# Kernel optimization log

Hardware: AMD Instinct MI355X
Metric: run time of the kernel (lower is better)

## Reference

```python
import jax, jax.numpy as jnp
import numpy as np

HEADS = 16
DIM_HEAD = 64
SCALE = DIM_HEAD ** -0.5


def setup_inputs() -> dict:
    key = jax.random.key(0)
    k1, k2, k3, k4 = jax.random.split(key, 4)
    b, n, dim = 4, 4096, 1024
    dim_inner = HEADS * DIM_HEAD
    x = jax.random.normal(k1, (b, n, dim), dtype=jnp.float32)
    W_qkv = jax.random.normal(k2, (dim, dim_inner * 3), dtype=jnp.float32) * 0.02
    agent_tokens = jax.random.normal(k3, (HEADS, 128, DIM_HEAD), dtype=jnp.float32) * 0.02
    W_out = jax.random.normal(k4, (dim_inner, dim), dtype=jnp.float32) * 0.02
    return {"x": x, "W_qkv": W_qkv, "agent_tokens": agent_tokens, "W_out": W_out}


def reference(x, W_qkv, agent_tokens, W_out):
    b, n, _ = x.shape
    h, m, d = agent_tokens.shape
    # qkv projection: b n (3 h d) -> 3, b, h, n, d
    qkv = (x @ W_qkv).reshape(b, n, 3, h, d).transpose(2, 0, 3, 1, 4)
    q, k, v = qkv[0], qkv[1], qkv[2]
    a = agent_tokens * SCALE  # h m d, broadcast over batch
    qa_sim = jnp.einsum('bhid,hjd->bhij', q, a)   # b h n m
    ak_sim = jnp.einsum('hid,bhjd->bhij', a, k)   # b h m n
    qa_attn = jax.nn.softmax(qa_sim, axis=-1)
    ak_attn = jax.nn.softmax(ak_sim, axis=-1)
    out = jnp.einsum('bhij,bhjd->bhid', ak_attn, v)    # b h m d
    out = jnp.einsum('bhij,bhjd->bhid', qa_attn, out)  # b h n d
    out = out.transpose(0, 2, 1, 3).reshape(b, n, h * d)
    return out @ W_out
```

## Files before the change

### kernel.cpp

```cpp
#include <hip/hip_runtime.h>

typedef __bf16 bf16x8 __attribute__((ext_vector_type(8)));
typedef float f32x4 __attribute__((ext_vector_type(4)));
typedef unsigned short ushort8 __attribute__((ext_vector_type(8)));
typedef unsigned short u16;

#define MFMA16(a, b, c) __builtin_amdgcn_mfma_f32_16x16x32_bf16(a, b, c, 0, 0, 0)
#define FENCE() __builtin_amdgcn_sched_barrier(0)
#define BARRIER() do { FENCE(); __builtin_amdgcn_s_barrier(); FENCE(); } while (0)
#define VMCNT(n) do { asm volatile("s_waitcnt vmcnt(" #n ")"); FENCE(); } while (0)

__device__ __forceinline__ u16 f2bf(float v) {
  unsigned int u = __builtin_bit_cast(unsigned int, v);
  u += 0x7fffu + ((u >> 16) & 1u);
  return (u16)(u >> 16);
}

__device__ __forceinline__ void gload16(const u16* g, u16* l) {
  __builtin_amdgcn_global_load_lds((__attribute__((address_space(1))) void*)(g),
                                   (__attribute__((address_space(3))) void*)(l), 16, 0, 0);
}

__global__ __launch_bounds__(256) void prep(const float* __restrict__ x, u16* __restrict__ x_bf,
                                            const float* __restrict__ Wqkv, u16* __restrict__ wqkvT,
                                            const float* __restrict__ Wout, u16* __restrict__ woutT,
                                            const float* __restrict__ agent, u16* __restrict__ a_bf) {
  __shared__ float tile[64][65];
  int bid = blockIdx.x;
  int t = threadIdx.x;
  if (bid < 8192) {
    size_t i = (size_t)bid * 256 + t;
    const float4* p = (const float4*)x + i * 2;
    float4 a = p[0], b = p[1];
    ushort8 o;
    o[0] = f2bf(a.x); o[1] = f2bf(a.y); o[2] = f2bf(a.z); o[3] = f2bf(a.w);
    o[4] = f2bf(b.x); o[5] = f2bf(b.y); o[6] = f2bf(b.z); o[7] = f2bf(b.w);
    *((ushort8*)x_bf + i) = o;
    return;
  }
  if (bid >= 9216) {
    int i = (bid - 9216) * 256 + t;
    a_bf[i] = f2bf(agent[i] * 0.125f);
    return;
  }
  const float* W; u16* WT; int K = 1024, N; int b2;
  if (bid < 8960) { W = Wqkv; WT = wqkvT; N = 3072; b2 = bid - 8192; }
  else            { W = Wout; WT = woutT; N = 1024; b2 = bid - 8960; }
  int nt = N >> 6;
  int kt = b2 / nt, nti = b2 - kt * nt;
  int k0 = kt << 6, n0 = nti << 6;
  int r = t >> 4, c4 = (t & 15) << 2;
#pragma unroll
  for (int j = 0; j < 4; ++j) {
    float4 v = *(const float4*)&W[(size_t)(k0 + j * 16 + r) * N + n0 + c4];
    tile[j * 16 + r][c4] = v.x; tile[j * 16 + r][c4 + 1] = v.y;
    tile[j * 16 + r][c4 + 2] = v.z; tile[j * 16 + r][c4 + 3] = v.w;
  }
  __syncthreads();
  int rn = t >> 2, cs = (t & 3) << 4;
  ushort8 o0, o1;
#pragma unroll
  for (int e = 0; e < 8; ++e) { o0[e] = f2bf(tile[cs + e][rn]); o1[e] = f2bf(tile[cs + 8 + e][rn]); }
  u16* dst = WT + (size_t)(n0 + rn) * K + k0 + cs;
  *(ushort8*)dst = o0;
  *(ushort8*)(dst + 8) = o1;
}

template <int MODE>
__global__ __launch_bounds__(512, 2) void gemm256(const u16* __restrict__ A, const u16* __restrict__ BT,
                                                  int M, int N, int K,
                                                  u16* __restrict__ qb, u16* __restrict__ kb,
                                                  u16* __restrict__ vt, float* __restrict__ outf) {
  extern __shared__ char smem[];
  const int NT = K >> 5;
  int ntiles = N >> 8;
  int nwg = (M >> 8) * ntiles;
  int bid = blockIdx.x;
  int wg = (bid & 7) * (nwg >> 3) + (bid >> 3);
  int tm = wg / ntiles, tn = wg - tm * ntiles;
  int rb = tm << 8, cb = tn << 8;
  int t = threadIdx.x;
  int w = t >> 6, lane = t & 63, li = lane & 15, lg = lane >> 4;
  int wr = w >> 2, wc = w & 3;

  const u16* srcA[2];
  const u16* srcB[2];
#pragma unroll
  for (int j = 0; j < 2; ++j) {
    int D = j * 8192 + t * 16;
    int L = D ^ (((D >> 7) & 3) << 4);
    int row = L >> 6, inb = L & 63;
    srcA[j] = A + (size_t)(rb + row) * K + (inb >> 1);
    srcB[j] = BT + (size_t)(cb + row) * K + (inb >> 1);
  }
#define STAGE_A(slot, kt) do { \
    gload16(srcA[0] + (kt) * 32, (u16*)(smem + (slot) * 32768 + t * 16)); \
    gload16(srcA[1] + (kt) * 32, (u16*)(smem + (slot) * 32768 + 8192 + t * 16)); } while (0)
#define STAGE_B(slot, kt) do { \
    gload16(srcB[0] + (kt) * 32, (u16*)(smem + (slot) * 32768 + 16384 + t * 16)); \
    gload16(srcB[1] + (kt) * 32, (u16*)(smem + (slot) * 32768 + 24576 + t * 16)); } while (0)

  int offA[8], offB[4];
#pragma unroll
  for (int m8 = 0; m8 < 8; ++m8) {
    int row = wr * 128 + m8 * 16 + li;
    int L = row * 64 + lg * 16;
    offA[m8] = L ^ (((L >> 7) & 3) << 4);
  }
#pragma unroll
  for (int n = 0; n < 4; ++n) {
    int row = wc * 64 + n * 16 + li;
    int L = row * 64 + lg * 16;
    offB[n] = 16384 + (L ^ (((L >> 7) & 3) << 4));
  }

  f32x4 acc[8][4];
#pragma unroll
  for (int m = 0; m < 8; ++m)
#pragma unroll
    for (int n = 0; n < 4; ++n) acc[m][n] = (f32x4){0.f, 0.f, 0.f, 0.f};

  bf16x8 aF[4], aS[4], b0[4], b1[4];

#define RD_A_LO(sb, d) do { d[0] = *(const bf16x8*)((sb) + offA[0]); d[1] = *(const bf16x8*)((sb) + offA[1]); \
                            d[2] = *(const bf16x8*)((sb) + offA[2]); d[3] = *(const bf16x8*)((sb) + offA[3]); } while (0)
#define RD_A_HI(sb, d) do { d[0] = *(const bf16x8*)((sb) + offA[4]); d[1] = *(const bf16x8*)((sb) + offA[5]); \
                            d[2] = *(const bf16x8*)((sb) + offA[6]); d[3] = *(const bf16x8*)((sb) + offA[7]); } while (0)
#define RD_B(sb, d)    do { d[0] = *(const bf16x8*)((sb) + offB[0]); d[1] = *(const bf16x8*)((sb) + offB[1]); \
                            d[2] = *(const bf16x8*)((sb) + offB[2]); d[3] = *(const bf16x8*)((sb) + offB[3]); } while (0)

#define PH_EVEN(t, BC, STG) do { \
    BARRIER(); \
    { char* sb_ = smem + ((t) & 3) * 32768; RD_A_HI(sb_, aS); } \
    if (STG) STAGE_A(((t) + 3) & 3, (t) + 3); \
    FENCE(); \
    __builtin_amdgcn_s_setprio(1); \
    _Pragma("unroll") for (int m = 0; m < 4; ++m) \
      _Pragma("unroll") for (int n = 0; n < 4; ++n) acc[m][n] = MFMA16(aF[m], BC[n], acc[m][n]); \
    __builtin_amdgcn_s_setprio(0); \
  } while (0)

#define PH_ODD(t, BC, BN, STG, RDNEXT, WAITOP) do { \
    WAITOP; \
    BARRIER(); \
    if (RDNEXT) { char* sb_ = smem + (((t) + 1) & 3) * 32768; RD_A_LO(sb_, aF); RD_B(sb_, BN); } \
    if (STG) STAGE_B(((t) + 3) & 3, (t) + 3); \
    FENCE(); \
    __builtin_amdgcn_s_setprio(1); \
    _Pragma("unroll") for (int m = 0; m < 4; ++m) \
      _Pragma("unroll") for (int n = 0; n < 4; ++n) acc[4 + m][n] = MFMA16(aS[m], BC[n], acc[4 + m][n]); \
    __builtin_amdgcn_s_setprio(0); \
  } while (0)

#define TILE(t, BC, BN, STG, RDNEXT, WAITOP) do { \
    PH_EVEN(t, BC, STG); \
    PH_ODD(t, BC, BN, STG, RDNEXT, WAITOP); \
  } while (0)

  STAGE_A(0, 0); STAGE_B(0, 0);
  STAGE_A(1, 1); STAGE_B(1, 1);
  STAGE_A(2, 2); STAGE_B(2, 2);
  VMCNT(8);
  BARRIER();
  RD_A_LO(smem, aF); RD_B(smem, b0);

  for (int tt = 0; tt <= NT - 6; tt += 2) {
    TILE(tt,     b0, b1, 1, 1, VMCNT(6));
    TILE(tt + 1, b1, b0, 1, 1, VMCNT(6));
  }
  TILE(NT - 4, b0, b1, 1, 1, VMCNT(6));
  TILE(NT - 3, b1, b0, 0, 1, VMCNT(4));
  TILE(NT - 2, b0, b1, 0, 1, VMCNT(0));
  TILE(NT - 1, b1, b0, 0, 0, ((void)0));

  if (MODE == 0) {
    int col0 = cb + wc * 64;
    int s = col0 >> 10;
    int hh = (col0 >> 6) & 15;
    if (s < 2) {
      u16* dst = (s == 0) ? qb : kb;
#pragma unroll
      for (int m = 0; m < 8; ++m) {
        int rbase = rb + wr * 128 + m * 16 + lg * 4;
#pragma unroll
        for (int r = 0; r < 4; ++r) {
          int rr = rbase + r;
          size_t o = (((size_t)(rr >> 12) * 16 + hh) * 4096 + (rr & 4095)) * 64;
#pragma unroll
          for (int n = 0; n < 4; ++n) dst[o + n * 16 + li] = f2bf(acc[m][n][r]);
        }
      }
    } else {
      BARRIER();
#pragma unroll
      for (int m = 0; m < 8; ++m) {
        int rl = wr * 128 + m * 16 + lg * 4;
#pragma unroll
        for (int n = 0; n < 4; ++n) {
          int colL = wc * 64 + n * 16 + li;
          unsigned int lo = (unsigned int)f2bf(acc[m][n][0]) | ((unsigned int)f2bf(acc[m][n][1]) << 16);
          unsigned int hi = (unsigned int)f2bf(acc[m][n][2]) | ((unsigned int)f2bf(acc[m][n][3]) << 16);
          int byte = (colL * 512 + rl * 2) ^ ((colL & 7) << 4);
          *(uint2*)(smem + byte) = make_uint2(lo, hi);
        }
      }
      BARRIER();
      int bb = rb >> 12, nnb = rb & 4095;
      int hh0b = (cb >> 6) & 15;
#pragma unroll
      for (int it = 0; it < 16; ++it) {
        int c = (it & 3) * 64 + w * 8 + (lane >> 3);
        int k = (it >> 2) * 8 + (lane & 7);
        int kk = (k & ~7) | ((k & 7) ^ (c & 7));
        uint4 v = *(const uint4*)(smem + c * 512 + kk * 16);
        size_t off = (((size_t)bb * 16 + hh0b + (c >> 6)) * 64 + (c & 63)) * 4096 + nnb + k * 8;
        *(uint4*)(vt + off) = v;
      }
    }
  } else {
#pragma unroll
    for (int m = 0; m < 8; ++m) {
#pragma unroll
      for (int r = 0; r < 4; ++r) {
        float* po = outf + (size_t)(rb + wr * 128 + m * 16 + lg * 4 + r) * N + cb + wc * 64;
#pragma unroll
        for (int n = 0; n < 4; ++n) po[n * 16 + li] = acc[m][n][r];
      }
    }
  }
#undef TILE
#undef PH_ODD
#undef PH_EVEN
#undef RD_A_LO
#undef RD_A_HI
#undef RD_B
#undef STAGE_A
#undef STAGE_B
}

__global__ __launch_bounds__(256) void ak_flash(const u16* __restrict__ kb, const u16* __restrict__ vt,
                                                const u16* __restrict__ ab,
                                                float* __restrict__ pO, float* __restrict__ pM,
                                                float* __restrict__ pL) {
  __shared__ u16 p_lds[128][136];
  int bid = blockIdx.x;
  int s = bid & 7;
  int bh = bid >> 3;
  int h = bh & 15;
  int t = threadIdx.x, w = t >> 6, l = t & 63, lg = l >> 4, li = l & 15;
  int jb = w * 32;

  bf16x8 afr[2][2];
#pragma unroll
  for (int jt = 0; jt < 2; ++jt)
#pragma unroll
    for (int kk = 0; kk < 2; ++kk)
      afr[jt][kk] = *(const bf16x8*)&ab[(size_t)(h * 128 + jb + jt * 16 + li) * 64 + kk * 32 + lg * 8];

  f32x4 O[2][4];
  float mrow[2][4], lrow[2][4];
#pragma unroll
  for (int jt = 0; jt < 2; ++jt) {
#pragma unroll
    for (int dt = 0; dt < 4; ++dt) O[jt][dt] = (f32x4){0.f, 0.f, 0.f, 0.f};
#pragma unroll
    for (int r = 0; r < 4; ++r) { mrow[jt][r] = -1e30f; lrow[jt][r] = 0.f; }
  }
  const u16* kbase = kb + (size_t)bh * 4096 * 64;
  const u16* vbase = vt + (size_t)bh * 64 * 4096;

  for (int c = 0; c < 4; ++c) {
    int i0 = s * 512 + c * 128;
    f32x4 sf[2][8];
#pragma unroll
    for (int jt = 0; jt < 2; ++jt)
#pragma unroll
      for (int it = 0; it < 8; ++it) sf[jt][it] = (f32x4){0.f, 0.f, 0.f, 0.f};
#pragma unroll
    for (int it = 0; it < 8; ++it)
#pragma unroll
      for (int kk = 0; kk < 2; ++kk) {
        bf16x8 bfr = *(const bf16x8*)&kbase[(size_t)(i0 + it * 16 + li) * 64 + kk * 32 + lg * 8];
        sf[0][it] = MFMA16(afr[0][kk], bfr, sf[0][it]);
        sf[1][it] = MFMA16(afr[1][kk], bfr, sf[1][it]);
      }
#pragma unroll
    for (int jt = 0; jt < 2; ++jt)
#pragma unroll
      for (int r = 0; r < 4; ++r) {
        float cm = sf[jt][0][r];
#pragma unroll
        for (int it = 1; it < 8; ++it) cm = fmaxf(cm, sf[jt][it][r]);
#pragma unroll
        for (int off = 1; off < 16; off <<= 1) cm = fmaxf(cm, __shfl_xor(cm, off));
        float mold = mrow[jt][r];
        float mnew = fmaxf(mold, cm);
        float scale = __expf(mold - mnew);
        float ss = 0.f;
#pragma unroll
        for (int it = 0; it < 8; ++it) {
          float p = __expf(sf[jt][it][r] - mnew);
          sf[jt][it][r] = p;
          ss += p;
        }
#pragma unroll
        for (int off = 1; off < 16; off <<= 1) ss += __shfl_xor(ss, off);
        lrow[jt][r] = lrow[jt][r] * scale + ss;
        mrow[jt][r] = mnew;
#pragma unroll
        for (int dt = 0; dt < 4; ++dt) O[jt][dt][r] *= scale;
      }
#pragma unroll
    for (int jt = 0; jt < 2; ++jt)
#pragma unroll
      for (int it = 0; it < 8; ++it)
#pragma unroll
        for (int r = 0; r < 4; ++r)
          p_lds[jb + jt * 16 + lg * 4 + r][it * 16 + li] = f2bf(sf[jt][it][r]);
#pragma unroll
    for (int ks = 0; ks < 4; ++ks) {
      bf16x8 pa0 = *(const bf16x8*)&p_lds[jb + li][ks * 32 + lg * 8];
      bf16x8 pa1 = *(const bf16x8*)&p_lds[jb + 16 + li][ks * 32 + lg * 8];
#pragma unroll
      for (int dt = 0; dt < 4; ++dt) {
        bf16x8 bv = *(const bf16x8*)&vbase[(size_t)(dt * 16 + li) * 4096 + i0 + ks * 32 + lg * 8];
        O[0][dt] = MFMA16(pa0, bv, O[0][dt]);
        O[1][dt] = MFMA16(pa1, bv, O[1][dt]);
      }
    }
  }
  size_t pb = ((size_t)bh * 8 + s) * 128;
#pragma unroll
  for (int jt = 0; jt < 2; ++jt)
#pragma unroll
    for (int dt = 0; dt < 4; ++dt)
#pragma unroll
      for (int r = 0; r < 4; ++r) {
        int j = jb + jt * 16 + lg * 4 + r;
        pO[(pb + j) * 64 + dt * 16 + li] = O[jt][dt][r];
      }
  if (li == 0) {
#pragma unroll
    for (int jt = 0; jt < 2; ++jt)
#pragma unroll
      for (int r = 0; r < 4; ++r) {
        int j = jb + jt * 16 + lg * 4 + r;
        pM[pb + j] = mrow[jt][r];
        pL[pb + j] = lrow[jt][r];
      }
  }
}

__global__ __launch_bounds__(128) void ak_combine(const float* __restrict__ pO, const float* __restrict__ pM,
                                                  const float* __restrict__ pL, u16* __restrict__ out1t) {
  int bh = blockIdx.x >> 3, dc = blockIdx.x & 7;
  int j = threadIdx.x;
  float ms[8], wv[8];
  float M = -1e30f;
#pragma unroll
  for (int s = 0; s < 8; ++s) { ms[s] = pM[((size_t)bh * 8 + s) * 128 + j]; M = fmaxf(M, ms[s]); }
  float L = 0.f;
#pragma unroll
  for (int s = 0; s < 8; ++s) { wv[s] = __expf(ms[s] - M); L += wv[s] * pL[((size_t)bh * 8 + s) * 128 + j]; }
  float inv = 1.f / L;
  float4 A = {0.f, 0.f, 0.f, 0.f}, B = {0.f, 0.f, 0.f, 0.f};
#pragma unroll
  for (int s = 0; s < 8; ++s) {
    const float4* p = (const float4*)&pO[(((size_t)bh * 8 + s) * 128 + j) * 64 + dc * 8];
    float4 x = p[0], y = p[1];
    A.x += wv[s] * x.x; A.y += wv[s] * x.y; A.z += wv[s] * x.z; A.w += wv[s] * x.w;
    B.x += wv[s] * y.x; B.y += wv[s] * y.y; B.z += wv[s] * y.z; B.w += wv[s] * y.w;
  }
  size_t ob = ((size_t)bh * 64 + dc * 8) * 128 + j;
  out1t[ob + 0 * 128] = f2bf(A.x * inv);
  out1t[ob + 1 * 128] = f2bf(A.y * inv);
  out1t[ob + 2 * 128] = f2bf(A.z * inv);
  out1t[ob + 3 * 128] = f2bf(A.w * inv);
  out1t[ob + 4 * 128] = f2bf(B.x * inv);
  out1t[ob + 5 * 128] = f2bf(B.y * inv);
  out1t[ob + 6 * 128] = f2bf(B.z * inv);
  out1t[ob + 7 * 128] = f2bf(B.w * inv);
}

__global__ __launch_bounds__(256) void qa_fused(const u16* __restrict__ qb, const u16* __restrict__ out1t,
                                                const u16* __restrict__ ab, u16* __restrict__ out2) {
  __shared__ u16 p_lds[128][136];
  int bid = blockIdx.x;
  int nt = bid & 31;
  int bh = bid >> 5;
  int h = bh & 15, b = bh >> 4;
  int t = threadIdx.x, w = t >> 6, l = t & 63, lg = l >> 4, li = l & 15;
  int n0 = nt * 128;

  const u16* qbase = qb + ((size_t)bh * 4096 + n0 + w * 32) * 64;
  bf16x8 qf[2][2];
#pragma unroll
  for (int rt = 0; rt < 2; ++rt)
#pragma unroll
    for (int kk = 0; kk < 2; ++kk)
      qf[rt][kk] = *(const bf16x8*)&qbase[(size_t)(rt * 16 + li) * 64 + kk * 32 + lg * 8];

  f32x4 sf[2][8];
#pragma unroll
  for (int rt = 0; rt < 2; ++rt)
#pragma unroll
    for (int jt = 0; jt < 8; ++jt) sf[rt][jt] = (f32x4){0.f, 0.f, 0.f, 0.f};

  const u16* abase = ab + h * 128 * 64;
#pragma unroll
  for (int jt = 0; jt < 8; ++jt)
#pragma unroll
    for (int kk = 0; kk < 2; ++kk) {
      bf16x8 bfr = *(const bf16x8*)&abase[(size_t)(jt * 16 + li) * 64 + kk * 32 + lg * 8];
      sf[0][jt] = MFMA16(qf[0][kk], bfr, sf[0][jt]);
      sf[1][jt] = MFMA16(qf[1][kk], bfr, sf[1][jt]);
    }
  float inv[2][4];
#pragma unroll
  for (int rt = 0; rt < 2; ++rt)
#pragma unroll
    for (int r = 0; r < 4; ++r) {
      float cm = sf[rt][0][r];
#pragma unroll
      for (int jt = 1; jt < 8; ++jt) cm = fmaxf(cm, sf[rt][jt][r]);
#pragma unroll
      for (int off = 1; off < 16; off <<= 1) cm = fmaxf(cm, __shfl_xor(cm, off));
      float ss = 0.f;
#pragma unroll
      for (int jt = 0; jt < 8; ++jt) {
        float p = __expf(sf[rt][jt][r] - cm);
        sf[rt][jt][r] = p;
        ss += p;
      }
#pragma unroll
      for (int off = 1; off < 16; off <<= 1) ss += __shfl_xor(ss, off);
      inv[rt][r] = 1.f / ss;
    }
#pragma unroll
  for (int rt = 0; rt < 2; ++rt)
#pragma unroll
    for (int jt = 0; jt < 8; ++jt)
#pragma unroll
      for (int r = 0; r < 4; ++r)
        p_lds[w * 32 + rt * 16 + lg * 4 + r][jt * 16 + li] = f2bf(sf[rt][jt][r]);

  f32x4 O[2][4];
#pragma unroll
  for (int rt = 0; rt < 2; ++rt)
#pragma unroll
    for (int dt = 0; dt < 4; ++dt) O[rt][dt] = (f32x4){0.f, 0.f, 0.f, 0.f};

  const u16* obase = out1t + (size_t)bh * 64 * 128;
#pragma unroll
  for (int ks = 0; ks < 4; ++ks) {
    bf16x8 pa0 = *(const bf16x8*)&p_lds[w * 32 + li][ks * 32 + lg * 8];
    bf16x8 pa1 = *(const bf16x8*)&p_lds[w * 32 + 16 + li][ks * 32 + lg * 8];
#pragma unroll
    for (int dt = 0; dt < 4; ++dt) {
      bf16x8 bv = *(const bf16x8*)&obase[(size_t)(dt * 16 + li) * 128 + ks * 32 + lg * 8];
      O[0][dt] = MFMA16(pa0, bv, O[0][dt]);
      O[1][dt] = MFMA16(pa1, bv, O[1][dt]);
    }
  }
#pragma unroll
  for (int rt = 0; rt < 2; ++rt)
#pragma unroll
    for (int dt = 0; dt < 4; ++dt)
#pragma unroll
      for (int r = 0; r < 4; ++r) {
        int nn = n0 + w * 32 + rt * 16 + lg * 4 + r;
        int col = h * 64 + dt * 16 + li;
        out2[((size_t)b * 4096 + nn) * 1024 + col] = f2bf(O[rt][dt][r] * inv[rt][r]);
      }
}

extern "C" void kernel_launch(void* const* d_in, const int* in_sizes, int n_in,
                              void* d_out, int out_size, void* d_ws, size_t ws_size,
                              hipStream_t stream) {
  const float* x = (const float*)d_in[0];
  const float* Wqkv = (const float*)d_in[1];
  const float* agent = (const float*)d_in[2];
  const float* Wout = (const float*)d_in[3];
  float* out = (float*)d_out;

  char* ws = (char*)d_ws;
  u16* x_bf  = (u16*)(ws + 0);
  u16* wqkvT = (u16*)(ws + 33554432);
  u16* woutT = (u16*)(ws + 39845888);
  u16* a_bf  = (u16*)(ws + 41943040);
  u16* qb    = (u16*)(ws + 42205184);
  u16* kb    = (u16*)(ws + 75759616);
  u16* vt    = (u16*)(ws + 142868480);
  float* pO  = (float*)(ws + 176422912);
  float* pM  = (float*)(ws + 193200128);
  float* pL  = (float*)(ws + 193724416);
  u16* out1t = (u16*)(ws + 194248704);
  u16* out2  = x_bf;

  (void)hipFuncSetAttribute((const void*)gemm256<0>, hipFuncAttributeMaxDynamicSharedMemorySize, 131072);
  (void)hipFuncSetAttribute((const void*)gemm256<1>, hipFuncAttributeMaxDynamicSharedMemorySize, 131072);

  prep<<<9728, 256, 0, stream>>>(x, x_bf, Wqkv, wqkvT, Wout, woutT, agent, a_bf);
  gemm256<0><<<768, 512, 131072, stream>>>(x_bf, wqkvT, 16384, 3072, 1024, qb, kb, vt, nullptr);
  ak_flash<<<512, 256, 0, stream>>>(kb, vt, a_bf, pO, pM, pL);
  ak_combine<<<512, 128, 0, stream>>>(pO, pM, pL, out1t);
  qa_fused<<<2048, 256, 0, stream>>>(qb, out1t, a_bf, out2);
  gemm256<1><<<256, 512, 131072, stream>>>(out2, woutT, 16384, 1024, 1024, nullptr, nullptr, nullptr, out);
}
```

Before: 279.1 us.

## Replace ping-pong two-phase GEMM main loop with single-barrier per-tile body

The GEMM main loop previously split each K tile into two phases, each with its own barrier and s_setprio, and prefetched the next tile's A-low and B fragments into double-buffered registers. Now each tile issues both global stages, reads all fragments from LDS, runs all 32 MFMAs, then waits and synchronises once. This halves barriers per tile and drops one register fragment buffer, aiming to cut sync overhead and register pressure. In exchange, LDS reads are no longer overlapped with the previous tile's MFMAs, so latency may be exposed and the wave-priority scheduling is lost.

New measurement: 285.7 us. +2.3%, slower.

```diff
diff --git a/kernel.cpp b/kernel.cpp
--- a/kernel.cpp
+++ b/kernel.cpp
@@ -8,7 +8,7 @@
 #define MFMA16(a, b, c) __builtin_amdgcn_mfma_f32_16x16x32_bf16(a, b, c, 0, 0, 0)
 #define FENCE() __builtin_amdgcn_sched_barrier(0)
 #define BARRIER() do { FENCE(); __builtin_amdgcn_s_barrier(); FENCE(); } while (0)
-#define VMCNT(n) do { asm volatile("s_waitcnt vmcnt(" #n ")"); FENCE(); } while (0)
+#define VMCNT(n) do { FENCE(); asm volatile("s_waitcnt vmcnt(" #n ")"); FENCE(); } while (0)
 
 __device__ __forceinline__ u16 f2bf(float v) {
   unsigned int u = __builtin_bit_cast(unsigned int, v);
@@ -120,7 +120,7 @@
 #pragma unroll
     for (int n = 0; n < 4; ++n) acc[m][n] = (f32x4){0.f, 0.f, 0.f, 0.f};
 
-  bf16x8 aF[4], aS[4], b0[4], b1[4];
+  bf16x8 aF[4], aS[4], bfr[4];
 
 #define RD_A_LO(sb, d) do { d[0] = *(const bf16x8*)((sb) + offA[0]); d[1] = *(const bf16x8*)((sb) + offA[1]); \
                             d[2] = *(const bf16x8*)((sb) + offA[2]); d[3] = *(const bf16x8*)((sb) + offA[3]); } while (0)
@@ -129,49 +129,30 @@
 #define RD_B(sb, d)    do { d[0] = *(const bf16x8*)((sb) + offB[0]); d[1] = *(const bf16x8*)((sb) + offB[1]); \
                             d[2] = *(const bf16x8*)((sb) + offB[2]); d[3] = *(const bf16x8*)((sb) + offB[3]); } while (0)
 
-#define PH_EVEN(t, BC, STG) do { \
-    BARRIER(); \
-    { char* sb_ = smem + ((t) & 3) * 32768; RD_A_HI(sb_, aS); } \
-    if (STG) STAGE_A(((t) + 3) & 3, (t) + 3); \
+#define GBODY(tt, STG, WAITOP) do { \
+    char* sb_ = smem + ((tt) & 3) * 32768; \
+    if (STG) { STAGE_A(((tt) + 3) & 3, (tt) + 3); STAGE_B(((tt) + 3) & 3, (tt) + 3); } \
+    RD_B(sb_, bfr); RD_A_LO(sb_, aF); RD_A_HI(sb_, aS); \
+    _Pragma("unroll") for (int m = 0; m < 4; ++m) \
+      _Pragma("unroll") for (int n = 0; n < 4; ++n) acc[m][n] = MFMA16(aF[m], bfr[n], acc[m][n]); \
+    _Pragma("unroll") for (int m = 0; m < 4; ++m) \
+      _Pragma("unroll") for (int n = 0; n < 4; ++n) acc[4 + m][n] = MFMA16(aS[m], bfr[n], acc[4 + m][n]); \
+    WAITOP; \
+    __builtin_amdgcn_s_barrier(); \
     FENCE(); \
-    __builtin_amdgcn_s_setprio(1); \
-    _Pragma("unroll") for (int m = 0; m < 4; ++m) \
-      _Pragma("unroll") for (int n = 0; n < 4; ++n) acc[m][n] = MFMA16(aF[m], BC[n], acc[m][n]); \
-    __builtin_amdgcn_s_setprio(0); \
-  } while (0)
-
-#define PH_ODD(t, BC, BN, STG, RDNEXT, WAITOP) do { \
-    WAITOP; \
-    BARRIER(); \
-    if (RDNEXT) { char* sb_ = smem + (((t) + 1) & 3) * 32768; RD_A_LO(sb_, aF); RD_B(sb_, BN); } \
-    if (STG) STAGE_B(((t) + 3) & 3, (t) + 3); \
-    FENCE(); \
-    __builtin_amdgcn_s_setprio(1); \
-    _Pragma("unroll") for (int m = 0; m < 4; ++m) \
-      _Pragma("unroll") for (int n = 0; n < 4; ++n) acc[4 + m][n] = MFMA16(aS[m], BC[n], acc[4 + m][n]); \
-    __builtin_amdgcn_s_setprio(0); \
-  } while (0)
-
-#define TILE(t, BC, BN, STG, RDNEXT, WAITOP) do { \
-    PH_EVEN(t, BC, STG); \
-    PH_ODD(t, BC, BN, STG, RDNEXT, WAITOP); \
   } while (0)
 
   STAGE_A(0, 0); STAGE_B(0, 0);
   STAGE_A(1, 1); STAGE_B(1, 1);
   STAGE_A(2, 2); STAGE_B(2, 2);
   VMCNT(8);
-  BARRIER();
-  RD_A_LO(smem, aF); RD_B(smem, b0);
-
-  for (int tt = 0; tt <= NT - 6; tt += 2) {
-    TILE(tt,     b0, b1, 1, 1, VMCNT(6));
-    TILE(tt + 1, b1, b0, 1, 1, VMCNT(6));
-  }
-  TILE(NT - 4, b0, b1, 1, 1, VMCNT(6));
-  TILE(NT - 3, b1, b0, 0, 1, VMCNT(4));
-  TILE(NT - 2, b0, b1, 0, 1, VMCNT(0));
-  TILE(NT - 1, b1, b0, 0, 0, ((void)0));
+  __builtin_amdgcn_s_barrier();
+  FENCE();
+
+  for (int tt = 0; tt < NT - 3; ++tt) GBODY(tt, 1, VMCNT(8));
+  GBODY(NT - 3, 0, VMCNT(4));
+  GBODY(NT - 2, 0, VMCNT(0));
+  GBODY(NT - 1, 0, ((void)0));
 
   if (MODE == 0) {
     int col0 = cb + wc * 64;
@@ -228,9 +209,7 @@
       }
     }
   }
-#undef TILE
-#undef PH_ODD
-#undef PH_EVEN
+#undef GBODY
 #undef RD_A_LO
 #undef RD_A_HI
 #undef RD_B
```

## Load GEMM B fragments directly from global into registers, bypassing LDS

Applied to the files above, without the earlier changes.

The GEMM kernel stops staging the B (weight) tile through shared memory. Each wave now loads its B fragments straight from global memory into registers, one k-tile ahead. This halves the LDS footprint per stage and removes B's LDS writes and reads. In exchange, each wave issues uncoalesced-ish global loads that waves sharing the same columns duplicate, which relies on cache hits, and the vmcnt accounting changes. The workspace layout is also compacted, moving pO into a gap.

Result: slower. 348.0 us (+24.7%).

```diff
diff --git a/kernel.cpp b/kernel.cpp
--- a/kernel.cpp
+++ b/kernel.cpp
@@ -84,35 +84,34 @@
   int wr = w >> 2, wc = w & 3;
 
   const u16* srcA[2];
-  const u16* srcB[2];
 #pragma unroll
   for (int j = 0; j < 2; ++j) {
     int D = j * 8192 + t * 16;
     int L = D ^ (((D >> 7) & 3) << 4);
     int row = L >> 6, inb = L & 63;
     srcA[j] = A + (size_t)(rb + row) * K + (inb >> 1);
-    srcB[j] = BT + (size_t)(cb + row) * K + (inb >> 1);
   }
 #define STAGE_A(slot, kt) do { \
-    gload16(srcA[0] + (kt) * 32, (u16*)(smem + (slot) * 32768 + t * 16)); \
-    gload16(srcA[1] + (kt) * 32, (u16*)(smem + (slot) * 32768 + 8192 + t * 16)); } while (0)
-#define STAGE_B(slot, kt) do { \
-    gload16(srcB[0] + (kt) * 32, (u16*)(smem + (slot) * 32768 + 16384 + t * 16)); \
-    gload16(srcB[1] + (kt) * 32, (u16*)(smem + (slot) * 32768 + 24576 + t * 16)); } while (0)
-
-  int offA[8], offB[4];
+    gload16(srcA[0] + (kt) * 32, (u16*)(smem + (slot) * 16384 + t * 16)); \
+    gload16(srcA[1] + (kt) * 32, (u16*)(smem + (slot) * 16384 + 8192 + t * 16)); } while (0)
+
+  const u16* bptr[4];
+#pragma unroll
+  for (int n = 0; n < 4; ++n)
+    bptr[n] = BT + (size_t)(cb + wc * 64 + n * 16 + li) * K + lg * 8;
+#define LDB(dst, tt) do { \
+    dst[0] = *(const bf16x8*)(bptr[0] + (tt) * 32); \
+    dst[1] = *(const bf16x8*)(bptr[1] + (tt) * 32); \
+    dst[2] = *(const bf16x8*)(bptr[2] + (tt) * 32); \
+    dst[3] = *(const bf16x8*)(bptr[3] + (tt) * 32); } while (0)
+
+  int offA[8];
 #pragma unroll
   for (int m8 = 0; m8 < 8; ++m8) {
     int row = wr * 128 + m8 * 16 + li;
     int L = row * 64 + lg * 16;
     offA[m8] = L ^ (((L >> 7) & 3) << 4);
   }
-#pragma unroll
-  for (int n = 0; n < 4; ++n) {
-    int row = wc * 64 + n * 16 + li;
-    int L = row * 64 + lg * 16;
-    offB[n] = 16384 + (L ^ (((L >> 7) & 3) << 4));
-  }
 
   f32x4 acc[8][4];
 #pragma unroll
@@ -126,13 +125,12 @@
                             d[2] = *(const bf16x8*)((sb) + offA[2]); d[3] = *(const bf16x8*)((sb) + offA[3]); } while (0)
 #define RD_A_HI(sb, d) do { d[0] = *(const bf16x8*)((sb) + offA[4]); d[1] = *(const bf16x8*)((sb) + offA[5]); \
                             d[2] = *(const bf16x8*)((sb) + offA[6]); d[3] = *(const bf16x8*)((sb) + offA[7]); } while (0)
-#define RD_B(sb, d)    do { d[0] = *(const bf16x8*)((sb) + offB[0]); d[1] = *(const bf16x8*)((sb) + offB[1]); \
-                            d[2] = *(const bf16x8*)((sb) + offB[2]); d[3] = *(const bf16x8*)((sb) + offB[3]); } while (0)
-
-#define PH_EVEN(t, BC, STG) do { \
+
+#define PH_EVEN(t, BC, BN, STG, LDBN) do { \
     BARRIER(); \
-    { char* sb_ = smem + ((t) & 3) * 32768; RD_A_HI(sb_, aS); } \
+    { char* sb_ = smem + ((t) & 3) * 16384; RD_A_HI(sb_, aS); } \
     if (STG) STAGE_A(((t) + 3) & 3, (t) + 3); \
+    if (LDBN) LDB(BN, (t) + 1); \
     FENCE(); \
     __builtin_amdgcn_s_setprio(1); \
     _Pragma("unroll") for (int m = 0; m < 4; ++m) \
@@ -140,11 +138,10 @@
     __builtin_amdgcn_s_setprio(0); \
   } while (0)
 
-#define PH_ODD(t, BC, BN, STG, RDNEXT, WAITOP) do { \
+#define PH_ODD(t, BC, RDNEXT, WAITOP) do { \
     WAITOP; \
     BARRIER(); \
-    if (RDNEXT) { char* sb_ = smem + (((t) + 1) & 3) * 32768; RD_A_LO(sb_, aF); RD_B(sb_, BN); } \
-    if (STG) STAGE_B(((t) + 3) & 3, (t) + 3); \
+    if (RDNEXT) { char* sb_ = smem + (((t) + 1) & 3) * 16384; RD_A_LO(sb_, aF); } \
     FENCE(); \
     __builtin_amdgcn_s_setprio(1); \
     _Pragma("unroll") for (int m = 0; m < 4; ++m) \
@@ -152,26 +149,27 @@
     __builtin_amdgcn_s_setprio(0); \
   } while (0)
 
-#define TILE(t, BC, BN, STG, RDNEXT, WAITOP) do { \
-    PH_EVEN(t, BC, STG); \
-    PH_ODD(t, BC, BN, STG, RDNEXT, WAITOP); \
+#define TILE(t, BC, BN, STG, LDBN, RDNEXT, WAITOP) do { \
+    PH_EVEN(t, BC, BN, STG, LDBN); \
+    PH_ODD(t, BC, RDNEXT, WAITOP); \
   } while (0)
 
-  STAGE_A(0, 0); STAGE_B(0, 0);
-  STAGE_A(1, 1); STAGE_B(1, 1);
-  STAGE_A(2, 2); STAGE_B(2, 2);
+  STAGE_A(0, 0);
+  STAGE_A(1, 1);
+  STAGE_A(2, 2);
+  LDB(b0, 0);
   VMCNT(8);
   BARRIER();
-  RD_A_LO(smem, aF); RD_B(smem, b0);
-
-  for (int tt = 0; tt <= NT - 6; tt += 2) {
-    TILE(tt,     b0, b1, 1, 1, VMCNT(6));
-    TILE(tt + 1, b1, b0, 1, 1, VMCNT(6));
-  }
-  TILE(NT - 4, b0, b1, 1, 1, VMCNT(6));
-  TILE(NT - 3, b1, b0, 0, 1, VMCNT(4));
-  TILE(NT - 2, b0, b1, 0, 1, VMCNT(0));
-  TILE(NT - 1, b1, b0, 0, 0, ((void)0));
+  RD_A_LO(smem, aF);
+
+  for (int tt = 0; tt <= NT - 5; tt += 2) {
+    TILE(tt,     b0, b1, 1, 1, 1, VMCNT(6));
+    TILE(tt + 1, b1, b0, 1, 1, 1, VMCNT(6));
+  }
+  TILE(NT - 4, b0, b1, 1, 1, 1, VMCNT(6));
+  TILE(NT - 3, b1, b0, 0, 1, 1, VMCNT(6));
+  TILE(NT - 2, b0, b1, 0, 1, 1, VMCNT(4));
+  TILE(NT - 1, b1, b0, 0, 0, 0, ((void)0));
 
   if (MODE == 0) {
     int col0 = cb + wc * 64;
@@ -233,9 +231,8 @@
 #undef PH_EVEN
 #undef RD_A_LO
 #undef RD_A_HI
-#undef RD_B
+#undef LDB
 #undef STAGE_A
-#undef STAGE_B
 }
 
 __global__ __launch_bounds__(256) void ak_flash(const u16* __restrict__ kb, const u16* __restrict__ vt,
@@ -490,11 +487,11 @@
   u16* a_bf  = (u16*)(ws + 41943040);
   u16* qb    = (u16*)(ws + 42205184);
   u16* kb    = (u16*)(ws + 75759616);
+  float* pO  = (float*)(ws + 109314048);
   u16* vt    = (u16*)(ws + 142868480);
-  float* pO  = (float*)(ws + 176422912);
-  float* pM  = (float*)(ws + 193200128);
-  float* pL  = (float*)(ws + 193724416);
-  u16* out1t = (u16*)(ws + 194248704);
+  float* pM  = (float*)(ws + 176422912);
+  float* pL  = (float*)(ws + 176947200);
+  u16* out1t = (u16*)(ws + 177471488);
   u16* out2  = x_bf;
 
   (void)hipFuncSetAttribute((const void*)gemm256<0>, hipFuncAttributeMaxDynamicSharedMemorySize, 131072);
```
